# Performance work log

Measured on AMD Instinct MI355X. Metric: run time of the kernel, lower is better.

The kernel has to match this reference:

```python
import jax, jax.numpy as jnp
from jax import lax
import numpy as np

DN = ('NCHW', 'OIHW', 'NCHW')

def _leaky(x):
    return jnp.where(x > 0, x, 0.2 * x)

def _forward(texts, styles, conv1_w, conv1_b, conv2_w, conv2_b, proj_w, proj_b,
             v1_w, v1_b, v2_w, v2_b, v3_w, v3_b, d1_w, d1_b, d2_w, d2_b):
    bs, tot, W, H = texts.shape
    C = proj_w.shape[1]  # style_channels
    # stack text/style as 2-channel images: [bs*tot, 2, W, H]
    ts = jnp.stack((texts, styles), axis=2).reshape(bs * tot, 2, W, H)
    # transnet: conv -> leaky -> conv -> leaky -> GAP -> linear
    x = lax.conv_general_dilated(ts, conv1_w, (2, 2), 'SAME', dimension_numbers=DN)
    x = _leaky(x + conv1_b[None, :, None, None])
    x = lax.conv_general_dilated(x, conv2_w, (2, 2), 'SAME', dimension_numbers=DN)
    x = _leaky(x + conv2_b[None, :, None, None])
    x = x.mean(axis=(2, 3))                              # [bs*tot, 64]
    feats = (x @ proj_w + proj_b).reshape(bs, tot, C)     # [bs, tot, C]
    # vec2vec scorer MLP -> tanh score per option
    h = _leaky(feats @ v1_w + v1_b)
    h = _leaky(h @ v2_w + v2_b)
    score = jnp.tanh(h @ v3_w + v3_b)[..., 0]             # [bs, tot]
    # top-1 routing: argmax + gather of the selected style vector
    idx = jnp.argmax(score, axis=1)                       # [bs]
    res = jnp.take_along_axis(feats, idx[:, None, None], axis=1)[:, 0]  # [bs, C]
    # vec2im decoder: MLP -> image [bs, 1, W, H]
    img = jnp.tanh(_leaky(res @ d1_w + d1_b) @ d2_w + d2_b)
    return img.reshape(bs, 1, W, H)

def setup_inputs() -> dict:
    key = jax.random.key(0)
    ks = jax.random.split(key, 12)
    bs, tot, W, H = 32, 64, 64, 64
    C, C1, C2, NFC, DH = 128, 32, 64, 128, 512
    s = 0.05
    def rn(k, shape):
        return jax.random.normal(k, shape, dtype=jnp.float32) * s
    return {
        'texts': jax.random.normal(ks[0], (bs, tot, W, H), dtype=jnp.float32),
        'styles': jax.random.normal(ks[1], (bs, tot, W, H), dtype=jnp.float32),
        'conv1_w': rn(ks[2], (C1, 2, 3, 3)),
        'conv1_b': jnp.zeros((C1,), jnp.float32),
        'conv2_w': rn(ks[3], (C2, C1, 3, 3)),
        'conv2_b': jnp.zeros((C2,), jnp.float32),
        'proj_w': rn(ks[4], (C2, C)),
        'proj_b': jnp.zeros((C,), jnp.float32),
        'v1_w': rn(ks[5], (C, NFC)),
        'v1_b': jnp.zeros((NFC,), jnp.float32),
        'v2_w': rn(ks[6], (NFC, NFC)),
        'v2_b': jnp.zeros((NFC,), jnp.float32),
        'v3_w': rn(ks[7], (NFC, 1)),
        'v3_b': jnp.zeros((1,), jnp.float32),
        'd1_w': rn(ks[8], (C, DH)),
        'd1_b': jnp.zeros((DH,), jnp.float32),
        'd2_w': rn(ks[9], (DH, W * H)),
        'd2_b': jnp.zeros((W * H,), jnp.float32),
    }

def reference(texts, styles, conv1_w, conv1_b, conv2_w, conv2_b, proj_w, proj_b,
              v1_w, v1_b, v2_w, v2_b, v3_w, v3_b, d1_w, d1_b, d2_w, d2_b):
    return _forward(texts, styles, conv1_w, conv1_b, conv2_w, conv2_b, proj_w, proj_b,
                    v1_w, v1_b, v2_w, v2_b, v3_w, v3_b, d1_w, d1_b, d2_w, d2_b)
```

## Files before the change

kernel.cpp:

```cpp
#include <hip/hip_runtime.h>
#include <cstddef>
#include <cstdint>

#define LEAKY(x) ((x) > 0.f ? (x) : 0.2f*(x))

typedef _Float16 f16x8  __attribute__((ext_vector_type(8)));
typedef float    f32x4  __attribute__((ext_vector_type(4)));
typedef float    f32x16 __attribute__((ext_vector_type(16)));

#define WS_FEATS   0
#define WS_SCORES  262144
#define WS_RES     264192
#define WS_W2      268288
#define WS_W1M     287744
#define WS_GAPP    288768

__global__ void kPack(const float* __restrict__ c1w, const float* __restrict__ c2w,
                      float* __restrict__ ws)
{
    _Float16* W2 = (_Float16*)(ws + WS_W2);
    _Float16* W1 = (_Float16*)(ws + WS_W1M);
    const int t = blockIdx.x*256 + threadIdx.x;
    for (int i = t; i < 2*64*152; i += 16*256) {
        int k = i % 152, rest = i / 152;
        int co = rest & 63, c = rest >> 6;
        _Float16 h = (_Float16)0.f, lo = (_Float16)0.f;
        if (k < 144) {
            int tap = k >> 4, cil = k & 15;
            float wv = c2w[(co*32 + c*16 + cil)*9 + tap];
            h  = (_Float16)wv;
            lo = (_Float16)(wv - (float)h);
        }
        W2[((size_t)(c*2 + 0)*64 + co)*152 + k] = h;
        W2[((size_t)(c*2 + 1)*64 + co)*152 + k] = lo;
    }
    if (t < 2048) {
        int pl = t >> 10, rest = t & 1023;
        int co = rest >> 5, k = rest & 31;
        int kh = k >> 3, j = k & 7, kw = j >> 1, ci = j & 1;
        float wv = 0.f;
        if (kh < 3 && kw < 3) wv = c1w[co*18 + ci*9 + kh*3 + kw];
        _Float16 hi = (_Float16)wv;
        W1[t] = pl ? (_Float16)(wv - (float)hi) : hi;
    }
}

__global__ __launch_bounds__(256) void kConv(
    const float* __restrict__ texts, const float* __restrict__ styles,
    const float* __restrict__ c1b, const float* __restrict__ c2b,
    const float* __restrict__ wsro, float* __restrict__ gapp)
{
    __shared__ __align__(16) union {
        _Float16 in[2][19][68][2];
        float    part[4][32];
    } s_u;
    __shared__ __align__(16) _Float16 s_x1[2][2][9][2][17][8];

    const int bid = blockIdx.x, tid = threadIdx.x;
    const int n = bid >> 2, q = bid & 3;
    const int w = tid >> 6, l = tid & 63;

    {
        const uint4 z4 = {0u,0u,0u,0u};
        uint4* z = (uint4*)&s_x1[0][0][0][0][0][0];
        for (int i = tid; i < 1224; i += 256) z[i] = z4;
        if (tid < 38) {
            int pl = tid >= 19, row = pl ? tid - 19 : tid;
            *(uint4*)&s_u.in[pl][row][64][0] = z4;
        }
    }
    for (int u = tid; u < 304; u += 256) {
        const int row = u >> 4, g = u & 15;
        const int grow = q*16 + row;
        float4 tv = {0.f,0.f,0.f,0.f}, sv = {0.f,0.f,0.f,0.f};
        if (grow < 64) {
            tv = *(const float4*)&texts [(size_t)n*4096 + grow*64 + g*4];
            sv = *(const float4*)&styles[(size_t)n*4096 + grow*64 + g*4];
        }
        float vals[8] = {tv.x, sv.x, tv.y, sv.y, tv.z, sv.z, tv.w, sv.w};
        _Float16 hh[8], ll[8];
        #pragma unroll
        for (int j = 0; j < 8; ++j) {
            _Float16 hi = (_Float16)vals[j];
            hh[j] = hi; ll[j] = (_Float16)(vals[j] - (float)hi);
        }
        *(uint4*)&s_u.in[0][row][g*4][0] = *(uint4*)hh;
        *(uint4*)&s_u.in[1][row][g*4][0] = *(uint4*)ll;
    }
    __syncthreads();

    const _Float16* W2h = (const _Float16*)(wsro + WS_W2);
    const _Float16* W1g = (const _Float16*)(wsro + WS_W1M);

    f32x16 acc;
    #pragma unroll
    for (int r = 0; r < 16; ++r) acc[r] = 0.f;

    const int mt = w >> 1, nh = w & 1;
    const int posl = mt*32 + (l & 31);
    const int py2 = posl >> 4, px2 = posl & 15;
    const int hf2 = l >> 5;
    const int co2 = nh*32 + (l & 31);
    const int kg = l >> 4, m16 = l & 15;
    const int NT = (q == 3) ? 16 : 18;

    for (int ch = 0; ch < 2; ++ch) {
        {
            f16x8 a_h = *(const f16x8*)&W1g[(0*32 + ch*16 + m16)*32 + kg*8];
            f16x8 a_l = *(const f16x8*)&W1g[(1*32 + ch*16 + m16)*32 + kg*8];
            float4 b4 = *(const float4*)&c1b[ch*16 + kg*4];
            for (int t = w; t < NT; t += 4) {
                const int py = t >> 1, px = (t & 1)*16 + m16;
                const int row = (kg < 3) ? (2*py + kg) : 0;
                const _Float16* bp0 = &s_u.in[0][row][2*px][0];
                const _Float16* bp1 = &s_u.in[1][row][2*px][0];
                f16x8 b_h, b_l;
                ((uint2*)&b_h)[0] = *(const uint2*)bp0;
                ((uint2*)&b_h)[1] = *(const uint2*)(bp0 + 4);
                ((uint2*)&b_l)[0] = *(const uint2*)bp1;
                ((uint2*)&b_l)[1] = *(const uint2*)(bp1 + 4);
                f32x4 c = {0.f,0.f,0.f,0.f};
                c = __builtin_amdgcn_mfma_f32_16x16x32_f16(a_l, b_h, c, 0, 0, 0);
                c = __builtin_amdgcn_mfma_f32_16x16x32_f16(a_h, b_l, c, 0, 0, 0);
                c = __builtin_amdgcn_mfma_f32_16x16x32_f16(a_h, b_h, c, 0, 0, 0);
                const int xp = px & 1, xq = px >> 1;
                _Float16 hh[4], ll[4];
                #pragma unroll
                for (int r = 0; r < 4; ++r) {
                    float v = c[r] + b4[r];
                    v = fmaxf(v, 0.2f*v);
                    _Float16 hi = (_Float16)v;
                    hh[r] = hi; ll[r] = (_Float16)(v - (float)hi);
                }
                *(uint2*)&s_x1[0][kg >> 1][py][xp][xq][(kg & 1)*4] = *(uint2*)hh;
                *(uint2*)&s_x1[1][kg >> 1][py][xp][xq][(kg & 1)*4] = *(uint2*)ll;
            }
        }
        __syncthreads();

        {
            const _Float16* Bg_h = W2h + ((size_t)(ch*2 + 0)*64 + co2)*152 + hf2*8;
            const _Float16* Bg_l = Bg_h + (size_t)64*152;
            #pragma unroll
            for (int tap = 0; tap < 9; ++tap) {
                const int kh = tap/3, kw = tap%3;
                const int xr = 2*px2 + kw;
                const int xp = xr & 1, xq = xr >> 1;
                const int r2 = 2*py2 + kh;
                f16x8 Ah = *(const f16x8*)&s_x1[0][hf2][r2][xp][xq][0];
                f16x8 Al = *(const f16x8*)&s_x1[1][hf2][r2][xp][xq][0];
                f16x8 Bh = *(const f16x8*)&Bg_h[tap*16];
                f16x8 Bl = *(const f16x8*)&Bg_l[tap*16];
                acc = __builtin_amdgcn_mfma_f32_32x32x16_f16(Ah, Bh, acc, 0, 0, 0);
                acc = __builtin_amdgcn_mfma_f32_32x32x16_f16(Al, Bh, acc, 0, 0, 0);
                acc = __builtin_amdgcn_mfma_f32_32x32x16_f16(Ah, Bl, acc, 0, 0, 0);
            }
        }
        __syncthreads();
    }

    {
        const float b2 = c2b[co2];
        float s = 0.f;
        #pragma unroll
        for (int r = 0; r < 16; ++r) {
            float v = acc[r] + b2;
            s += fmaxf(v, 0.2f*v);
        }
        s += __shfl_xor(s, 32);
        if (l < 32) s_u.part[w][l] = s;
    }
    __syncthreads();
    if (tid < 64) {
        const int nhc = tid >> 5, cl = tid & 31;
        float g = s_u.part[0*2 + nhc][cl] + s_u.part[1*2 + nhc][cl];
        gapp[(size_t)(n*4 + q)*64 + tid] = g;
    }
}

__global__ __launch_bounds__(128) void kScore(
    const float* __restrict__ gapp,
    const float* __restrict__ pw,  const float* __restrict__ pb,
    const float* __restrict__ v1w, const float* __restrict__ v1b,
    const float* __restrict__ v2w, const float* __restrict__ v2b,
    const float* __restrict__ v3w, const float* __restrict__ v3b,
    float* __restrict__ feats, float* __restrict__ scores)
{
    __shared__ float s_gap[64], s_f[128], s_h[128], s_red[2];
    const int n = blockIdx.x, tid = threadIdx.x;

    if (tid < 64) {
        const float* gp = &gapp[(size_t)n*256 + tid];
        s_gap[tid] = (gp[0] + gp[64] + gp[128] + gp[192]) * (1.f/256.f);
    }
    __syncthreads();
    {
        float a = pb[tid];
        #pragma unroll 8
        for (int m = 0; m < 64; ++m) a += s_gap[m]*pw[m*128 + tid];
        feats[(size_t)n*128 + tid] = a;
        s_f[tid] = a;
    }
    __syncthreads();
    {
        float a = v1b[tid];
        #pragma unroll 8
        for (int m = 0; m < 128; ++m) a += s_f[m]*v1w[m*128 + tid];
        s_h[tid] = LEAKY(a);
    }
    __syncthreads();
    {
        float a = v2b[tid];
        #pragma unroll 8
        for (int m = 0; m < 128; ++m) a += s_h[m]*v2w[m*128 + tid];
        a = LEAKY(a);
        s_f[tid] = a * v3w[tid];
    }
    __syncthreads();
    {
        float p = s_f[tid];
        #pragma unroll
        for (int off = 32; off; off >>= 1) p += __shfl_xor(p, off);
        if ((tid & 63) == 0) s_red[tid >> 6] = p;
    }
    __syncthreads();
    if (tid == 0) scores[n] = tanhf(s_red[0] + s_red[1] + v3b[0]);
}

__global__ __launch_bounds__(128) void kArgGather(
    const float* __restrict__ scores, const float* __restrict__ feats,
    float* __restrict__ res)
{
    __shared__ int s_idx;
    const int b = blockIdx.x, tid = threadIdx.x;
    if (tid < 64) {
        float v = scores[b*64 + tid];
        int   i = tid;
        #pragma unroll
        for (int off = 32; off; off >>= 1) {
            float ov = __shfl_xor(v, off);
            int   oi = __shfl_xor(i, off);
            if (ov > v || (ov == v && oi < i)) { v = ov; i = oi; }
        }
        if (tid == 0) s_idx = i;
    }
    __syncthreads();
    const int idx = s_idx;
    res[b*128 + tid] = feats[((size_t)b*64 + idx)*128 + tid];
}

__global__ __launch_bounds__(512) void kDecode(
    const float* __restrict__ res,
    const float* __restrict__ d1w, const float* __restrict__ d1b,
    const float* __restrict__ d2w, const float* __restrict__ d2b,
    float* __restrict__ out)
{
    __shared__ float s_res[128];
    __shared__ float s_h[512];
    const int bid = blockIdx.x;
    const int b = bid >> 3, ot = bid & 7;
    const int tid = threadIdx.x;

    if (tid < 128) s_res[tid] = res[b*128 + tid];
    __syncthreads();
    {
        float a = d1b[tid];
        #pragma unroll 8
        for (int m = 0; m < 128; ++m) a += s_res[m]*d1w[m*512 + tid];
        s_h[tid] = LEAKY(a);
    }
    __syncthreads();
    const int o = ot*512 + tid;
    float a = d2b[o];
    for (int k = 0; k < 512; k += 4) {
        float4 h4 = *(const float4*)&s_h[k];
        a += h4.x*d2w[(size_t)(k+0)*4096 + o];
        a += h4.y*d2w[(size_t)(k+1)*4096 + o];
        a += h4.z*d2w[(size_t)(k+2)*4096 + o];
        a += h4.w*d2w[(size_t)(k+3)*4096 + o];
    }
    out[(size_t)b*4096 + o] = tanhf(a);
}

extern "C" void kernel_launch(void* const* d_in, const int* in_sizes, int n_in,
                              void* d_out, int out_size, void* d_ws, size_t ws_size,
                              hipStream_t stream)
{
    const float* texts  = (const float*)d_in[0];
    const float* styles = (const float*)d_in[1];
    const float* c1w = (const float*)d_in[2];
    const float* c1b = (const float*)d_in[3];
    const float* c2w = (const float*)d_in[4];
    const float* c2b = (const float*)d_in[5];
    const float* pw  = (const float*)d_in[6];
    const float* pb  = (const float*)d_in[7];
    const float* v1w = (const float*)d_in[8];
    const float* v1b = (const float*)d_in[9];
    const float* v2w = (const float*)d_in[10];
    const float* v2b = (const float*)d_in[11];
    const float* v3w = (const float*)d_in[12];
    const float* v3b = (const float*)d_in[13];
    const float* d1w = (const float*)d_in[14];
    const float* d1b = (const float*)d_in[15];
    const float* d2w = (const float*)d_in[16];
    const float* d2b = (const float*)d_in[17];

    float* ws     = (float*)d_ws;
    float* feats  = ws + WS_FEATS;
    float* scores = ws + WS_SCORES;
    float* res    = ws + WS_RES;
    float* gapp   = ws + WS_GAPP;

    kPack<<<dim3(16), dim3(256), 0, stream>>>(c1w, c2w, ws);
    kConv<<<dim3(8192), dim3(256), 0, stream>>>(
        texts, styles, c1b, c2b, (const float*)ws, gapp);
    kScore<<<dim3(2048), dim3(128), 0, stream>>>(
        gapp, pw, pb, v1w, v1b, v2w, v2b, v3w, v3b, feats, scores);
    kArgGather<<<dim3(32), dim3(128), 0, stream>>>(scores, feats, res);
    kDecode<<<dim3(256), dim3(512), 0, stream>>>(res, d1w, d1b, d2w, d2b,
                                                 (float*)d_out);
}
```

Baseline: 140.0 us.

## Double-buffer conv1 output to cut barriers and fuse argmax into decoder

The conv kernel now writes conv1 output into two shared-memory buffers, one per channel half. This drops the barrier between the channel iterations and lets conv1 for the second half run alongside conv2 for the first half. The argmax+gather kernel is folded into the decoder, so every decode block recomputes the argmax and reads the selected feature directly, removing one launch and the res round trip. The cost is doubled s_x1 shared memory, which may lower occupancy in the 8192-block conv kernel, plus redundant argmax work across the 8 decoder blocks per batch.

```diff
diff --git a/kernel.cpp b/kernel.cpp
--- a/kernel.cpp
+++ b/kernel.cpp
@@ -10,7 +10,6 @@
 
 #define WS_FEATS   0
 #define WS_SCORES  262144
-#define WS_RES     264192
 #define WS_W2      268288
 #define WS_W1M     287744
 #define WS_GAPP    288768
@@ -54,7 +53,7 @@
         _Float16 in[2][19][68][2];
         float    part[4][32];
     } s_u;
-    __shared__ __align__(16) _Float16 s_x1[2][2][9][2][17][8];
+    __shared__ __align__(16) _Float16 s_x1[2][2][2][9][2][17][8];
 
     const int bid = blockIdx.x, tid = threadIdx.x;
     const int n = bid >> 2, q = bid & 3;
@@ -62,8 +61,8 @@
 
     {
         const uint4 z4 = {0u,0u,0u,0u};
-        uint4* z = (uint4*)&s_x1[0][0][0][0][0][0];
-        for (int i = tid; i < 1224; i += 256) z[i] = z4;
+        uint4* z = (uint4*)&s_x1[0][0][0][0][0][0][0];
+        for (int i = tid; i < 2448; i += 256) z[i] = z4;
         if (tid < 38) {
             int pl = tid >= 19, row = pl ? tid - 19 : tid;
             *(uint4*)&s_u.in[pl][row][64][0] = z4;
@@ -104,60 +103,63 @@
     const int kg = l >> 4, m16 = l & 15;
     const int NT = (q == 3) ? 16 : 18;
 
-    for (int ch = 0; ch < 2; ++ch) {
-        {
-            f16x8 a_h = *(const f16x8*)&W1g[(0*32 + ch*16 + m16)*32 + kg*8];
-            f16x8 a_l = *(const f16x8*)&W1g[(1*32 + ch*16 + m16)*32 + kg*8];
-            float4 b4 = *(const float4*)&c1b[ch*16 + kg*4];
-            for (int t = w; t < NT; t += 4) {
-                const int py = t >> 1, px = (t & 1)*16 + m16;
-                const int row = (kg < 3) ? (2*py + kg) : 0;
-                const _Float16* bp0 = &s_u.in[0][row][2*px][0];
-                const _Float16* bp1 = &s_u.in[1][row][2*px][0];
-                f16x8 b_h, b_l;
-                ((uint2*)&b_h)[0] = *(const uint2*)bp0;
-                ((uint2*)&b_h)[1] = *(const uint2*)(bp0 + 4);
-                ((uint2*)&b_l)[0] = *(const uint2*)bp1;
-                ((uint2*)&b_l)[1] = *(const uint2*)(bp1 + 4);
-                f32x4 c = {0.f,0.f,0.f,0.f};
-                c = __builtin_amdgcn_mfma_f32_16x16x32_f16(a_l, b_h, c, 0, 0, 0);
-                c = __builtin_amdgcn_mfma_f32_16x16x32_f16(a_h, b_l, c, 0, 0, 0);
-                c = __builtin_amdgcn_mfma_f32_16x16x32_f16(a_h, b_h, c, 0, 0, 0);
-                const int xp = px & 1, xq = px >> 1;
-                _Float16 hh[4], ll[4];
-                #pragma unroll
-                for (int r = 0; r < 4; ++r) {
-                    float v = c[r] + b4[r];
-                    v = fmaxf(v, 0.2f*v);
-                    _Float16 hi = (_Float16)v;
-                    hh[r] = hi; ll[r] = (_Float16)(v - (float)hi);
-                }
-                *(uint2*)&s_x1[0][kg >> 1][py][xp][xq][(kg & 1)*4] = *(uint2*)hh;
-                *(uint2*)&s_x1[1][kg >> 1][py][xp][xq][(kg & 1)*4] = *(uint2*)ll;
+    auto conv1 = [&](int ch, int buf) {
+        f16x8 a_h = *(const f16x8*)&W1g[(0*32 + ch*16 + m16)*32 + kg*8];
+        f16x8 a_l = *(const f16x8*)&W1g[(1*32 + ch*16 + m16)*32 + kg*8];
+        float4 b4 = *(const float4*)&c1b[ch*16 + kg*4];
+        for (int t = w; t < NT; t += 4) {
+            const int py = t >> 1, px = (t & 1)*16 + m16;
+            const int row = (kg < 3) ? (2*py + kg) : 0;
+            const _Float16* bp0 = &s_u.in[0][row][2*px][0];
+            const _Float16* bp1 = &s_u.in[1][row][2*px][0];
+            f16x8 b_h, b_l;
+            ((uint2*)&b_h)[0] = *(const uint2*)bp0;
+            ((uint2*)&b_h)[1] = *(const uint2*)(bp0 + 4);
+            ((uint2*)&b_l)[0] = *(const uint2*)bp1;
+            ((uint2*)&b_l)[1] = *(const uint2*)(bp1 + 4);
+            f32x4 c = {0.f,0.f,0.f,0.f};
+            c = __builtin_amdgcn_mfma_f32_16x16x32_f16(a_l, b_h, c, 0, 0, 0);
+            c = __builtin_amdgcn_mfma_f32_16x16x32_f16(a_h, b_l, c, 0, 0, 0);
+            c = __builtin_amdgcn_mfma_f32_16x16x32_f16(a_h, b_h, c, 0, 0, 0);
+            const int xp = px & 1, xq = px >> 1;
+            _Float16 hh[4], ll[4];
+            #pragma unroll
+            for (int r = 0; r < 4; ++r) {
+                float v = c[r] + b4[r];
+                v = fmaxf(v, 0.2f*v);
+                _Float16 hi = (_Float16)v;
+                hh[r] = hi; ll[r] = (_Float16)(v - (float)hi);
             }
-        }
-        __syncthreads();
-
-        {
-            const _Float16* Bg_h = W2h + ((size_t)(ch*2 + 0)*64 + co2)*152 + hf2*8;
-            const _Float16* Bg_l = Bg_h + (size_t)64*152;
-            #pragma unroll
-            for (int tap = 0; tap < 9; ++tap) {
-                const int kh = tap/3, kw = tap%3;
-                const int xr = 2*px2 + kw;
-                const int xp = xr & 1, xq = xr >> 1;
-                const int r2 = 2*py2 + kh;
-                f16x8 Ah = *(const f16x8*)&s_x1[0][hf2][r2][xp][xq][0];
-                f16x8 Al = *(const f16x8*)&s_x1[1][hf2][r2][xp][xq][0];
-                f16x8 Bh = *(const f16x8*)&Bg_h[tap*16];
-                f16x8 Bl = *(const f16x8*)&Bg_l[tap*16];
-                acc = __builtin_amdgcn_mfma_f32_32x32x16_f16(Ah, Bh, acc, 0, 0, 0);
-                acc = __builtin_amdgcn_mfma_f32_32x32x16_f16(Al, Bh, acc, 0, 0, 0);
-                acc = __builtin_amdgcn_mfma_f32_32x32x16_f16(Ah, Bl, acc, 0, 0, 0);
-            }
-        }
-        __syncthreads();
-    }
+            *(uint2*)&s_x1[buf][0][kg >> 1][py][xp][xq][(kg & 1)*4] = *(uint2*)hh;
+            *(uint2*)&s_x1[buf][1][kg >> 1][py][xp][xq][(kg & 1)*4] = *(uint2*)ll;
+        }
+    };
+
+    auto conv2 = [&](int ch, int buf) {
+        const _Float16* Bg_h = W2h + ((size_t)(ch*2 + 0)*64 + co2)*152 + hf2*8;
+        const _Float16* Bg_l = Bg_h + (size_t)64*152;
+        #pragma unroll
+        for (int tap = 0; tap < 9; ++tap) {
+            const int kh = tap/3, kw = tap%3;
+            const int xr = 2*px2 + kw;
+            const int xp = xr & 1, xq = xr >> 1;
+            const int r2 = 2*py2 + kh;
+            f16x8 Ah = *(const f16x8*)&s_x1[buf][0][hf2][r2][xp][xq][0];
+            f16x8 Al = *(const f16x8*)&s_x1[buf][1][hf2][r2][xp][xq][0];
+            f16x8 Bh = *(const f16x8*)&Bg_h[tap*16];
+            f16x8 Bl = *(const f16x8*)&Bg_l[tap*16];
+            acc = __builtin_amdgcn_mfma_f32_32x32x16_f16(Ah, Bh, acc, 0, 0, 0);
+            acc = __builtin_amdgcn_mfma_f32_32x32x16_f16(Al, Bh, acc, 0, 0, 0);
+            acc = __builtin_amdgcn_mfma_f32_32x32x16_f16(Ah, Bl, acc, 0, 0, 0);
+        }
+    };
+
+    conv1(0, 0);
+    __syncthreads();
+    conv1(1, 1);
+    conv2(0, 0);
+    __syncthreads();
+    conv2(1, 1);
 
     {
         const float b2 = c2b[co2];
@@ -227,12 +229,19 @@
     if (tid == 0) scores[n] = tanhf(s_red[0] + s_red[1] + v3b[0]);
 }
 
-__global__ __launch_bounds__(128) void kArgGather(
+__global__ __launch_bounds__(512) void kDecode(
     const float* __restrict__ scores, const float* __restrict__ feats,
-    float* __restrict__ res)
-{
+    const float* __restrict__ d1w, const float* __restrict__ d1b,
+    const float* __restrict__ d2w, const float* __restrict__ d2b,
+    float* __restrict__ out)
+{
+    __shared__ float s_res[128];
+    __shared__ float s_h[512];
     __shared__ int s_idx;
-    const int b = blockIdx.x, tid = threadIdx.x;
+    const int bid = blockIdx.x;
+    const int b = bid >> 3, ot = bid & 7;
+    const int tid = threadIdx.x;
+
     if (tid < 64) {
         float v = scores[b*64 + tid];
         int   i = tid;
@@ -245,23 +254,7 @@
         if (tid == 0) s_idx = i;
     }
     __syncthreads();
-    const int idx = s_idx;
-    res[b*128 + tid] = feats[((size_t)b*64 + idx)*128 + tid];
-}
-
-__global__ __launch_bounds__(512) void kDecode(
-    const float* __restrict__ res,
-    const float* __restrict__ d1w, const float* __restrict__ d1b,
-    const float* __restrict__ d2w, const float* __restrict__ d2b,
-    float* __restrict__ out)
-{
-    __shared__ float s_res[128];
-    __shared__ float s_h[512];
-    const int bid = blockIdx.x;
-    const int b = bid >> 3, ot = bid & 7;
-    const int tid = threadIdx.x;
-
-    if (tid < 128) s_res[tid] = res[b*128 + tid];
+    if (tid < 128) s_res[tid] = feats[((size_t)b*64 + s_idx)*128 + tid];
     __syncthreads();
     {
         float a = d1b[tid];
@@ -308,7 +301,6 @@
     float* ws     = (float*)d_ws;
     float* feats  = ws + WS_FEATS;
     float* scores = ws + WS_SCORES;
-    float* res    = ws + WS_RES;
     float* gapp   = ws + WS_GAPP;
 
     kPack<<<dim3(16), dim3(256), 0, stream>>>(c1w, c2w, ws);
@@ -316,7 +308,6 @@
         texts, styles, c1b, c2b, (const float*)ws, gapp);
     kScore<<<dim3(2048), dim3(128), 0, stream>>>(
         gapp, pw, pb, v1w, v1b, v2w, v2b, v3w, v3b, feats, scores);
-    kArgGather<<<dim3(32), dim3(128), 0, stream>>>(scores, feats, res);
-    kDecode<<<dim3(256), dim3(512), 0, stream>>>(res, d1w, d1b, d2w, d2b,
-                                                 (float*)d_out);
-}
+    kDecode<<<dim3(256), dim3(512), 0, stream>>>(
+        scores, feats, d1w, d1b, d2w, d2b, (float*)d_out);
+}
```

New measurement: 146.3 us. 4.6% more time.
